# Performance work log

Measured on AMD Instinct MI355X. Metric: run time of the kernel, lower is better.

The kernel has to match this reference:

```python
import jax, jax.numpy as jnp
import numpy as np

B, IN, OUT = 65536, 256, 256
EPS = 1e-10


def setup_inputs() -> dict:
    key = jax.random.key(0)
    k1, k2, k3 = jax.random.split(key, 3)
    x = jax.random.normal(k1, (B, IN), dtype=jnp.float32)
    # match nn.Linear default init scale roughly (kaiming-uniform-ish)
    W = jax.random.normal(k2, (OUT, IN), dtype=jnp.float32) / np.sqrt(IN)
    b = jax.random.normal(k3, (OUT,), dtype=jnp.float32) / np.sqrt(IN)
    return {"x": x, "W": W, "b": b}


def reference(x, W, b):
    # x: [B, in], W: [out, in], b: [out]
    # x_len[i] = sqrt(sum_k x[i,k]^2)  (original does x^2 @ ones^T -> same value per out col)
    x_len = jnp.sqrt(jnp.sum(x * x, axis=-1, keepdims=True))           # [B, 1]
    # w_len[j] = sqrt(sum_k W[j,k]^2)  (original does ones @ (W^2)^T -> same value per row)
    w_len = jnp.sqrt(jnp.sum(W * W, axis=-1))[None, :]                  # [1, out]
    x_len = jax.lax.stop_gradient(x_len)
    w_len = jax.lax.stop_gradient(w_len)
    b_sg = jax.lax.stop_gradient(b)
    out = x @ W.T + b                                                   # linear(x), grads flow
    out = out - b_sg[None, :]                                           # bias.data subtraction (no grad)
    out = jnp.maximum(out / (x_len * w_len), EPS)                       # cosine normalize + clamp
    out = out + b_sg[None, :]                                           # bias.data added back (no grad)
    return out
```

## Files before the change

kernel.cpp:

```cpp
#include <hip/hip_runtime.h>
#include <hip/hip_bf16.h>
#include <math.h>


using bf16x8 = __attribute__((ext_vector_type(8))) short;
using f32x4  = __attribute__((ext_vector_type(4))) float;

#define W_LDS_BYTES 131072
#define LDS_BYTES   (W_LDS_BYTES + 1024 + 1024)
#define EPS 1e-10f

__device__ __forceinline__ short f2bf(float f) {
    __bf16 h = (__bf16)f;
    return __builtin_bit_cast(short, h);
}

__global__ __launch_bounds__(1024, 4) void ffn_cosnorm_kernel(
    const float* __restrict__ x, const float* __restrict__ W,
    const float* __restrict__ b, float* __restrict__ out)
{
    extern __shared__ char smem[];
    float* winv = (float*)(smem + W_LDS_BYTES);
    float* blds = (float*)(smem + W_LDS_BYTES + 1024);

    const int t    = threadIdx.x;
    const int lane = t & 63;
    const int wave = t >> 6;
    const int r16  = lane & 15;
    const int kg   = lane >> 4;
    const int rxor = (r16 & 7) << 4;
    const size_t rowb = (size_t)blockIdx.x * 256 + (size_t)wave * 16;

    const float* xp = x + (rowb + r16) * 256 + kg * 8;

    float4 fa[8], fb[8];
    #pragma unroll
    for (int s = 0; s < 8; ++s) {
        fa[s] = *(const float4*)(xp + s * 32);
        fb[s] = *(const float4*)(xp + s * 32 + 4);
    }

    {
        const int wrow = t >> 2;
        const int q    = t & 3;
        const float* wr = W + (size_t)wrow * 256 + q * 64;
        const int rx = (wrow & 7) << 4;
        float ss = 0.f;
        #pragma unroll
        for (int i = 0; i < 8; ++i) {
            float4 a = *(const float4*)(wr + i * 8);
            float4 c = *(const float4*)(wr + i * 8 + 4);
            ss = fmaf(a.x, a.x, ss); ss = fmaf(a.y, a.y, ss);
            ss = fmaf(a.z, a.z, ss); ss = fmaf(a.w, a.w, ss);
            ss = fmaf(c.x, c.x, ss); ss = fmaf(c.y, c.y, ss);
            ss = fmaf(c.z, c.z, ss); ss = fmaf(c.w, c.w, ss);
            bf16x8 v;
            v[0] = f2bf(a.x); v[1] = f2bf(a.y); v[2] = f2bf(a.z); v[3] = f2bf(a.w);
            v[4] = f2bf(c.x); v[5] = f2bf(c.y); v[6] = f2bf(c.z); v[7] = f2bf(c.w);
            const int off = wrow * 512 + ((q * 128 + i * 16) ^ rx);
            *(bf16x8*)(smem + off) = v;
        }
        ss += __shfl_xor(ss, 1);
        ss += __shfl_xor(ss, 2);
        if (q == 0) winv[wrow] = 1.0f / sqrtf(ss);
        if (t < 256) blds[t] = b[t];
    }

    bf16x8 xb[8];
    float ssx = 0.f;
    #pragma unroll
    for (int s = 0; s < 8; ++s) {
        float4 a = fa[s], c = fb[s];
        bf16x8 v;
        v[0] = f2bf(a.x); v[1] = f2bf(a.y); v[2] = f2bf(a.z); v[3] = f2bf(a.w);
        v[4] = f2bf(c.x); v[5] = f2bf(c.y); v[6] = f2bf(c.z); v[7] = f2bf(c.w);
        xb[s] = v;
        ssx = fmaf(a.x, a.x, ssx); ssx = fmaf(a.y, a.y, ssx);
        ssx = fmaf(a.z, a.z, ssx); ssx = fmaf(a.w, a.w, ssx);
        ssx = fmaf(c.x, c.x, ssx); ssx = fmaf(c.y, c.y, ssx);
        ssx = fmaf(c.z, c.z, ssx); ssx = fmaf(c.w, c.w, ssx);
    }

    ssx += __shfl_xor(ssx, 16); ssx += __shfl_xor(ssx, 32);
    const float inv = 1.0f / sqrtf(ssx);

    __syncthreads();

    const int jb = kg * 4;
    float* op = out + (rowb + r16) * 256;

    #pragma unroll
    for (int n = 0; n < 16; ++n) {
        f32x4 acc = f32x4{0.f, 0.f, 0.f, 0.f};
        #pragma unroll
        for (int k0 = 0; k0 < 8; ++k0) {
            const int addr = (n * 16 + r16) * 512 + ((k0 * 64 + kg * 16) ^ rxor);
            bf16x8 wfr = *(const bf16x8*)(smem + addr);
            acc = __builtin_amdgcn_mfma_f32_16x16x32_bf16(wfr, xb[k0], acc, 0, 0, 0);
        }
        float4 wv = *(const float4*)(winv + n * 16 + jb);
        float4 bv = *(const float4*)(blds + n * 16 + jb);
        f32x4 o;
        o[0] = fmaxf(acc[0] * (inv * wv.x), EPS) + bv.x;
        o[1] = fmaxf(acc[1] * (inv * wv.y), EPS) + bv.y;
        o[2] = fmaxf(acc[2] * (inv * wv.z), EPS) + bv.z;
        o[3] = fmaxf(acc[3] * (inv * wv.w), EPS) + bv.w;
        *(f32x4*)(op + n * 16 + jb) = o;
        __builtin_amdgcn_sched_barrier(0);
    }
}

extern "C" void kernel_launch(void* const* d_in, const int* in_sizes, int n_in,
                              void* d_out, int out_size, void* d_ws, size_t ws_size,
                              hipStream_t stream) {
    const float* x = (const float*)d_in[0];
    const float* W = (const float*)d_in[1];
    const float* b = (const float*)d_in[2];
    float* out = (float*)d_out;

    hipFuncSetAttribute((const void*)ffn_cosnorm_kernel,
                        hipFuncAttributeMaxDynamicSharedMemorySize, LDS_BYTES);
    ffn_cosnorm_kernel<<<dim3(256), dim3(1024), LDS_BYTES, stream>>>(x, W, b, out);
}
```

Before: 34.63 us.

## Split W staging into two K-halves to halve LDS and double block count

Blocks shrink from 1024 to 512 threads covering 128 rows each, and the bf16 copy of W is staged in two 64 KB halves along K instead of one 128 KB buffer. The first half feeds 16 accumulators kept in registers, then the second half is loaded and the norms and epilogue run. The smaller LDS footprint should let more blocks share a CU and doubles the grid to 512 blocks. In exchange every block reads and converts W twice with extra barriers, and holding 16 accumulator vectors raises register pressure. Waves also start at rotated column tiles to spread LDS bank traffic.

```diff
diff --git a/kernel.cpp b/kernel.cpp
--- a/kernel.cpp
+++ b/kernel.cpp
@@ -6,7 +6,7 @@
 using bf16x8 = __attribute__((ext_vector_type(8))) short;
 using f32x4  = __attribute__((ext_vector_type(4))) float;
 
-#define W_LDS_BYTES 131072
+#define W_LDS_BYTES 65536
 #define LDS_BYTES   (W_LDS_BYTES + 1024 + 1024)
 #define EPS 1e-10f
 
@@ -15,7 +15,7 @@
     return __builtin_bit_cast(short, h);
 }
 
-__global__ __launch_bounds__(1024, 4) void ffn_cosnorm_kernel(
+__global__ __launch_bounds__(512, 4) void ffn_cosnorm_kernel(
     const float* __restrict__ x, const float* __restrict__ W,
     const float* __restrict__ b, float* __restrict__ out)
 {
@@ -29,7 +29,7 @@
     const int r16  = lane & 15;
     const int kg   = lane >> 4;
     const int rxor = (r16 & 7) << 4;
-    const size_t rowb = (size_t)blockIdx.x * 256 + (size_t)wave * 16;
+    const size_t rowb = (size_t)blockIdx.x * 128 + (size_t)wave * 16;
 
     const float* xp = x + (rowb + r16) * 256 + kg * 8;
 
@@ -41,8 +41,8 @@
     }
 
     {
-        const int wrow = t >> 2;
-        const int q    = t & 3;
+        const int wrow = t >> 1;
+        const int q    = t & 1;
         const float* wr = W + (size_t)wrow * 256 + q * 64;
         const int rx = (wrow & 7) << 4;
         float ss = 0.f;
@@ -57,13 +57,12 @@
             bf16x8 v;
             v[0] = f2bf(a.x); v[1] = f2bf(a.y); v[2] = f2bf(a.z); v[3] = f2bf(a.w);
             v[4] = f2bf(c.x); v[5] = f2bf(c.y); v[6] = f2bf(c.z); v[7] = f2bf(c.w);
-            const int off = wrow * 512 + ((q * 128 + i * 16) ^ rx);
+            const int off = wrow * 256 + ((q * 128 + i * 16) ^ rx);
             *(bf16x8*)(smem + off) = v;
         }
         ss += __shfl_xor(ss, 1);
-        ss += __shfl_xor(ss, 2);
-        if (q == 0) winv[wrow] = 1.0f / sqrtf(ss);
-        if (t < 256) blds[t] = b[t];
+        if (!q) winv[wrow] = ss;
+        else    blds[wrow] = b[wrow];
     }
 
     bf16x8 xb[8];
@@ -80,31 +79,72 @@
         ssx = fmaf(c.x, c.x, ssx); ssx = fmaf(c.y, c.y, ssx);
         ssx = fmaf(c.z, c.z, ssx); ssx = fmaf(c.w, c.w, ssx);
     }
-
     ssx += __shfl_xor(ssx, 16); ssx += __shfl_xor(ssx, 32);
     const float inv = 1.0f / sqrtf(ssx);
 
     __syncthreads();
 
+    f32x4 acc[16];
+    #pragma unroll
+    for (int i = 0; i < 16; ++i) {
+        const int n = (wave * 2 + i) & 15;
+        f32x4 a = f32x4{0.f, 0.f, 0.f, 0.f};
+        #pragma unroll
+        for (int k0 = 0; k0 < 4; ++k0) {
+            const int addr = (n * 16 + r16) * 256 + ((k0 * 64 + kg * 16) ^ rxor);
+            bf16x8 wfr = *(const bf16x8*)(smem + addr);
+            a = __builtin_amdgcn_mfma_f32_16x16x32_bf16(wfr, xb[k0], a, 0, 0, 0);
+        }
+        acc[i] = a;
+    }
+
+    __syncthreads();
+
+    {
+        const int wrow = t >> 1;
+        const int q    = t & 1;
+        const float* wr = W + (size_t)wrow * 256 + 128 + q * 64;
+        const int rx = (wrow & 7) << 4;
+        float ss = 0.f;
+        #pragma unroll
+        for (int i = 0; i < 8; ++i) {
+            float4 a = *(const float4*)(wr + i * 8);
+            float4 c = *(const float4*)(wr + i * 8 + 4);
+            ss = fmaf(a.x, a.x, ss); ss = fmaf(a.y, a.y, ss);
+            ss = fmaf(a.z, a.z, ss); ss = fmaf(a.w, a.w, ss);
+            ss = fmaf(c.x, c.x, ss); ss = fmaf(c.y, c.y, ss);
+            ss = fmaf(c.z, c.z, ss); ss = fmaf(c.w, c.w, ss);
+            bf16x8 v;
+            v[0] = f2bf(a.x); v[1] = f2bf(a.y); v[2] = f2bf(a.z); v[3] = f2bf(a.w);
+            v[4] = f2bf(c.x); v[5] = f2bf(c.y); v[6] = f2bf(c.z); v[7] = f2bf(c.w);
+            const int off = wrow * 256 + ((q * 128 + i * 16) ^ rx);
+            *(bf16x8*)(smem + off) = v;
+        }
+        ss += __shfl_xor(ss, 1);
+        if (!q) winv[wrow] = 1.0f / sqrtf(winv[wrow] + ss);
+    }
+
+    __syncthreads();
+
     const int jb = kg * 4;
     float* op = out + (rowb + r16) * 256;
-
     #pragma unroll
-    for (int n = 0; n < 16; ++n) {
-        f32x4 acc = f32x4{0.f, 0.f, 0.f, 0.f};
+    for (int i = 0; i < 16; ++i) {
+        const int n = (wave * 2 + i) & 15;
+        f32x4 a = acc[i];
         #pragma unroll
-        for (int k0 = 0; k0 < 8; ++k0) {
-            const int addr = (n * 16 + r16) * 512 + ((k0 * 64 + kg * 16) ^ rxor);
+        for (int k0 = 0; k0 < 4; ++k0) {
+            const int addr = (n * 16 + r16) * 256 + ((k0 * 64 + kg * 16) ^ rxor);
             bf16x8 wfr = *(const bf16x8*)(smem + addr);
-            acc = __builtin_amdgcn_mfma_f32_16x16x32_bf16(wfr, xb[k0], acc, 0, 0, 0);
+            a = __builtin_amdgcn_mfma_f32_16x16x32_bf16(wfr, xb[4 + k0], a, 0, 0, 0);
         }
         float4 wv = *(const float4*)(winv + n * 16 + jb);
         float4 bv = *(const float4*)(blds + n * 16 + jb);
         f32x4 o;
-        o[0] = fmaxf(acc[0] * (inv * wv.x), EPS) + bv.x;
-        o[1] = fmaxf(acc[1] * (inv * wv.y), EPS) + bv.y;
-        o[2] = fmaxf(acc[2] * (inv * wv.z), EPS) + bv.z;
-        o[3] = fmaxf(acc[3] * (inv * wv.w), EPS) + bv.w;
+        o[0] = fmaxf(a[0] * (inv * wv.x), EPS) + bv.x;
+        o[1] = fmaxf(a[1] * (inv * wv.y), EPS) + bv.y;
+        o[2] = fmaxf(a[2] * (inv * wv.z), EPS) + bv.z;
+        o[3] = fmaxf(a[3] * (inv * wv.w), EPS) + bv.w;
         *(f32x4*)(op + n * 16 + jb) = o;
         __builtin_amdgcn_sched_barrier(0);
     }
@@ -120,5 +160,5 @@
 
     hipFuncSetAttribute((const void*)ffn_cosnorm_kernel,
                         hipFuncAttributeMaxDynamicSharedMemorySize, LDS_BYTES);
-    ffn_cosnorm_kernel<<<dim3(256), dim3(1024), LDS_BYTES, stream>>>(x, W, b, out);
+    ffn_cosnorm_kernel<<<dim3(512), dim3(512), LDS_BYTES, stream>>>(x, W, b, out);
 }
```

Result: slower. 45.01 us (+30.0%).

## Keep W in registers and stream x through double-buffered LDS slabs

Applied to the files above, without the earlier changes.

Each wave now holds two 16-column W slices as bf16 fragments in registers, and the x rows stream through two 8 KB LDS slabs, prefetching the next 16-row slab while the current one is used for MFMA. The grid becomes 512 blocks of 512 threads covering 128 rows each, cutting LDS from about 130 KB to about 16 KB per block, which allows more resident blocks. In exchange, every block re-reads and re-converts its W slices from global memory, and each slab step adds a block-wide barrier.

```diff
diff --git a/kernel.cpp b/kernel.cpp
--- a/kernel.cpp
+++ b/kernel.cpp
@@ -6,8 +6,8 @@
 using bf16x8 = __attribute__((ext_vector_type(8))) short;
 using f32x4  = __attribute__((ext_vector_type(4))) float;
 
-#define W_LDS_BYTES 131072
-#define LDS_BYTES   (W_LDS_BYTES + 1024 + 1024)
+#define SLAB_BYTES 8192
+#define LDS_BYTES  (2 * SLAB_BYTES + 2 * 16 * 4)
 #define EPS 1e-10f
 
 __device__ __forceinline__ short f2bf(float f) {
@@ -15,13 +15,27 @@
     return __builtin_bit_cast(short, h);
 }
 
-__global__ __launch_bounds__(1024, 4) void ffn_cosnorm_kernel(
+__device__ __forceinline__ float sumsq8(float4 a, float4 c, float s) {
+    s = fmaf(a.x, a.x, s); s = fmaf(a.y, a.y, s);
+    s = fmaf(a.z, a.z, s); s = fmaf(a.w, a.w, s);
+    s = fmaf(c.x, c.x, s); s = fmaf(c.y, c.y, s);
+    s = fmaf(c.z, c.z, s); s = fmaf(c.w, c.w, s);
+    return s;
+}
+
+__device__ __forceinline__ bf16x8 pack8(float4 a, float4 c) {
+    bf16x8 v;
+    v[0] = f2bf(a.x); v[1] = f2bf(a.y); v[2] = f2bf(a.z); v[3] = f2bf(a.w);
+    v[4] = f2bf(c.x); v[5] = f2bf(c.y); v[6] = f2bf(c.z); v[7] = f2bf(c.w);
+    return v;
+}
+
+__global__ __launch_bounds__(512, 4) void ffn_cosnorm_kernel(
     const float* __restrict__ x, const float* __restrict__ W,
     const float* __restrict__ b, float* __restrict__ out)
 {
     extern __shared__ char smem[];
-    float* winv = (float*)(smem + W_LDS_BYTES);
-    float* blds = (float*)(smem + W_LDS_BYTES + 1024);
+    float* ssq = (float*)(smem + 2 * SLAB_BYTES);
 
     const int t    = threadIdx.x;
     const int lane = t & 63;
@@ -29,84 +43,100 @@
     const int r16  = lane & 15;
     const int kg   = lane >> 4;
     const int rxor = (r16 & 7) << 4;
-    const size_t rowb = (size_t)blockIdx.x * 256 + (size_t)wave * 16;
+    const size_t rowbase = (size_t)blockIdx.x * 128;
 
-    const float* xp = x + (rowb + r16) * 256 + kg * 8;
+    const int srow = t >> 5;
+    const int c2   = t & 31;
+    const int soff = srow * 512 + ((c2 * 16) ^ ((srow & 7) << 4));
+    const float* sp = x + (rowbase + srow) * 256 + c2 * 8;
 
-    float4 fa[8], fb[8];
-    #pragma unroll
-    for (int s = 0; s < 8; ++s) {
-        fa[s] = *(const float4*)(xp + s * 32);
-        fb[s] = *(const float4*)(xp + s * 32 + 4);
+    float4 g0 = *(const float4*)(sp);
+    float4 g1 = *(const float4*)(sp + 4);
+
+    bf16x8 xw0[8], xw1[8];
+    float wv0[4], wv1[4];
+    float4 bv0, bv1;
+    const int n0 = wave, n1 = wave + 8;
+    {
+        const float* wr0 = W + (size_t)(n0 * 16 + r16) * 256 + kg * 8;
+        const float* wr1 = W + (size_t)(n1 * 16 + r16) * 256 + kg * 8;
+        float s0 = 0.f, s1 = 0.f;
+        #pragma unroll
+        for (int k0 = 0; k0 < 8; ++k0) {
+            float4 a0 = *(const float4*)(wr0 + k0 * 32);
+            float4 c0 = *(const float4*)(wr0 + k0 * 32 + 4);
+            xw0[k0] = pack8(a0, c0);
+            s0 = sumsq8(a0, c0, s0);
+            float4 a1 = *(const float4*)(wr1 + k0 * 32);
+            float4 c1 = *(const float4*)(wr1 + k0 * 32 + 4);
+            xw1[k0] = pack8(a1, c1);
+            s1 = sumsq8(a1, c1, s1);
+        }
+        s0 += __shfl_xor(s0, 16); s0 += __shfl_xor(s0, 32);
+        s1 += __shfl_xor(s1, 16); s1 += __shfl_xor(s1, 32);
+        const float iw0 = 1.0f / sqrtf(s0);
+        const float iw1 = 1.0f / sqrtf(s1);
+        #pragma unroll
+        for (int r = 0; r < 4; ++r) {
+            wv0[r] = __shfl(iw0, kg * 4 + r);
+            wv1[r] = __shfl(iw1, kg * 4 + r);
+        }
+        bv0 = *(const float4*)(b + n0 * 16 + kg * 4);
+        bv1 = *(const float4*)(b + n1 * 16 + kg * 4);
     }
 
     {
-        const int wrow = t >> 2;
-        const int q    = t & 3;
-        const float* wr = W + (size_t)wrow * 256 + q * 64;
-        const int rx = (wrow & 7) << 4;
-        float ss = 0.f;
-        #pragma unroll
-        for (int i = 0; i < 8; ++i) {
-            float4 a = *(const float4*)(wr + i * 8);
-            float4 c = *(const float4*)(wr + i * 8 + 4);
-            ss = fmaf(a.x, a.x, ss); ss = fmaf(a.y, a.y, ss);
-            ss = fmaf(a.z, a.z, ss); ss = fmaf(a.w, a.w, ss);
-            ss = fmaf(c.x, c.x, ss); ss = fmaf(c.y, c.y, ss);
-            ss = fmaf(c.z, c.z, ss); ss = fmaf(c.w, c.w, ss);
-            bf16x8 v;
-            v[0] = f2bf(a.x); v[1] = f2bf(a.y); v[2] = f2bf(a.z); v[3] = f2bf(a.w);
-            v[4] = f2bf(c.x); v[5] = f2bf(c.y); v[6] = f2bf(c.z); v[7] = f2bf(c.w);
-            const int off = wrow * 512 + ((q * 128 + i * 16) ^ rx);
-            *(bf16x8*)(smem + off) = v;
-        }
-        ss += __shfl_xor(ss, 1);
-        ss += __shfl_xor(ss, 2);
-        if (q == 0) winv[wrow] = 1.0f / sqrtf(ss);
-        if (t < 256) blds[t] = b[t];
+        float sp2 = sumsq8(g0, g1, 0.f);
+        *(bf16x8*)(smem + soff) = pack8(g0, g1);
+        sp2 += __shfl_xor(sp2, 1);  sp2 += __shfl_xor(sp2, 2);
+        sp2 += __shfl_xor(sp2, 4);  sp2 += __shfl_xor(sp2, 8);
+        sp2 += __shfl_xor(sp2, 16);
+        if ((lane & 31) == 0) ssq[srow] = sp2;
     }
-
-    bf16x8 xb[8];
-    float ssx = 0.f;
-    #pragma unroll
-    for (int s = 0; s < 8; ++s) {
-        float4 a = fa[s], c = fb[s];
-        bf16x8 v;
-        v[0] = f2bf(a.x); v[1] = f2bf(a.y); v[2] = f2bf(a.z); v[3] = f2bf(a.w);
-        v[4] = f2bf(c.x); v[5] = f2bf(c.y); v[6] = f2bf(c.z); v[7] = f2bf(c.w);
-        xb[s] = v;
-        ssx = fmaf(a.x, a.x, ssx); ssx = fmaf(a.y, a.y, ssx);
-        ssx = fmaf(a.z, a.z, ssx); ssx = fmaf(a.w, a.w, ssx);
-        ssx = fmaf(c.x, c.x, ssx); ssx = fmaf(c.y, c.y, ssx);
-        ssx = fmaf(c.z, c.z, ssx); ssx = fmaf(c.w, c.w, ssx);
-    }
-
-    ssx += __shfl_xor(ssx, 16); ssx += __shfl_xor(ssx, 32);
-    const float inv = 1.0f / sqrtf(ssx);
-
     __syncthreads();
 
-    const int jb = kg * 4;
-    float* op = out + (rowb + r16) * 256;
+    #pragma unroll
+    for (int i = 0; i < 8; ++i) {
+        const int cur = i & 1;
+        float4 h0, h1;
+        if (i < 7) {
+            const float* np = sp + (size_t)(i + 1) * 16 * 256;
+            h0 = *(const float4*)(np);
+            h1 = *(const float4*)(np + 4);
+        }
 
-    #pragma unroll
-    for (int n = 0; n < 16; ++n) {
-        f32x4 acc = f32x4{0.f, 0.f, 0.f, 0.f};
+        const float invx = 1.0f / sqrtf(ssq[cur * 16 + r16]);
+        f32x4 a0 = f32x4{0.f, 0.f, 0.f, 0.f};
+        f32x4 a1 = f32x4{0.f, 0.f, 0.f, 0.f};
         #pragma unroll
         for (int k0 = 0; k0 < 8; ++k0) {
-            const int addr = (n * 16 + r16) * 512 + ((k0 * 64 + kg * 16) ^ rxor);
-            bf16x8 wfr = *(const bf16x8*)(smem + addr);
-            acc = __builtin_amdgcn_mfma_f32_16x16x32_bf16(wfr, xb[k0], acc, 0, 0, 0);
+            bf16x8 bfr = *(const bf16x8*)(smem + cur * SLAB_BYTES +
+                                          r16 * 512 + ((k0 * 64 + kg * 16) ^ rxor));
+            a0 = __builtin_amdgcn_mfma_f32_16x16x32_bf16(xw0[k0], bfr, a0, 0, 0, 0);
+            a1 = __builtin_amdgcn_mfma_f32_16x16x32_bf16(xw1[k0], bfr, a1, 0, 0, 0);
         }
-        float4 wv = *(const float4*)(winv + n * 16 + jb);
-        float4 bv = *(const float4*)(blds + n * 16 + jb);
-        f32x4 o;
-        o[0] = fmaxf(acc[0] * (inv * wv.x), EPS) + bv.x;
-        o[1] = fmaxf(acc[1] * (inv * wv.y), EPS) + bv.y;
-        o[2] = fmaxf(acc[2] * (inv * wv.z), EPS) + bv.z;
-        o[3] = fmaxf(acc[3] * (inv * wv.w), EPS) + bv.w;
-        *(f32x4*)(op + n * 16 + jb) = o;
-        __builtin_amdgcn_sched_barrier(0);
+        float* op = out + (rowbase + i * 16 + r16) * 256;
+        f32x4 o0, o1;
+        o0[0] = fmaxf(a0[0] * (invx * wv0[0]), EPS) + bv0.x;
+        o0[1] = fmaxf(a0[1] * (invx * wv0[1]), EPS) + bv0.y;
+        o0[2] = fmaxf(a0[2] * (invx * wv0[2]), EPS) + bv0.z;
+        o0[3] = fmaxf(a0[3] * (invx * wv0[3]), EPS) + bv0.w;
+        o1[0] = fmaxf(a1[0] * (invx * wv1[0]), EPS) + bv1.x;
+        o1[1] = fmaxf(a1[1] * (invx * wv1[1]), EPS) + bv1.y;
+        o1[2] = fmaxf(a1[2] * (invx * wv1[2]), EPS) + bv1.z;
+        o1[3] = fmaxf(a1[3] * (invx * wv1[3]), EPS) + bv1.w;
+        *(f32x4*)(op + n0 * 16 + kg * 4) = o0;
+        *(f32x4*)(op + n1 * 16 + kg * 4) = o1;
+
+        if (i < 7) {
+            float sp2 = sumsq8(h0, h1, 0.f);
+            *(bf16x8*)(smem + (cur ^ 1) * SLAB_BYTES + soff) = pack8(h0, h1);
+            sp2 += __shfl_xor(sp2, 1);  sp2 += __shfl_xor(sp2, 2);
+            sp2 += __shfl_xor(sp2, 4);  sp2 += __shfl_xor(sp2, 8);
+            sp2 += __shfl_xor(sp2, 16);
+            if ((lane & 31) == 0) ssq[(cur ^ 1) * 16 + srow] = sp2;
+        }
+        __syncthreads();
     }
 }
 
@@ -120,5 +150,5 @@
 
     hipFuncSetAttribute((const void*)ffn_cosnorm_kernel,
                         hipFuncAttributeMaxDynamicSharedMemorySize, LDS_BYTES);
-    ffn_cosnorm_kernel<<<dim3(256), dim3(1024), LDS_BYTES, stream>>>(x, W, b, out);
+    ffn_cosnorm_kernel<<<dim3(512), dim3(512), LDS_BYTES, stream>>>(x, W, b, out);
 }
```

Measured after the change: 50.47 us. 1.46x slower.

## Stage x tiles through LDS with async global_load_lds double buffering

Applied to the files above, without the earlier changes.

Replaces direct per-thread register loads of x with asynchronous global-to-LDS DMA into a per-wave slab, double-buffered in 64-column quarters with XOR swizzling. Each wave waits on vmcnt, converts the staged quarter to bf16 and accumulates the norm while the next quarter streams in. The W staging now runs after an extra barrier because the x slabs reuse the W region of LDS. The per-tile sched_barrier in the output loop is also removed. This adds a barrier and serialises the x and W phases in exchange for coalesced DMA and lower register pressure.

```diff
diff --git a/kernel.cpp b/kernel.cpp
--- a/kernel.cpp
+++ b/kernel.cpp
@@ -13,6 +13,13 @@
 __device__ __forceinline__ short f2bf(float f) {
     __bf16 h = (__bf16)f;
     return __builtin_bit_cast(short, h);
+}
+
+__device__ __forceinline__ void dma16(const float* g, char* l) {
+    __builtin_amdgcn_global_load_lds(
+        (const __attribute__((address_space(1))) void*)g,
+        (__attribute__((address_space(3))) void*)l,
+        16 , 0, 0);
 }
 
 __global__ __launch_bounds__(1024, 4) void ffn_cosnorm_kernel(
@@ -31,14 +38,62 @@
     const int rxor = (r16 & 7) << 4;
     const size_t rowb = (size_t)blockIdx.x * 256 + (size_t)wave * 16;
 
-    const float* xp = x + (rowb + r16) * 256 + kg * 8;
+    char* slab = smem + wave * 8192;
 
-    float4 fa[8], fb[8];
+    const int drow = lane >> 4;
+    const int dc   = lane & 15;
+
     #pragma unroll
-    for (int s = 0; s < 8; ++s) {
-        fa[s] = *(const float4*)(xp + s * 32);
-        fb[s] = *(const float4*)(xp + s * 32 + 4);
+    for (int q = 0; q < 2; ++q) {
+        #pragma unroll
+        for (int j = 0; j < 4; ++j) {
+            const int row16 = j * 4 + drow;
+            const float* g = x + (rowb + row16) * 256 + q * 64
+                               + ((dc ^ (row16 & 7)) << 2);
+            dma16(g, slab + (q & 1) * 4096 + j * 1024);
+        }
     }
+
+    bf16x8 xb[8];
+    float ssx = 0.f;
+    #pragma unroll
+    for (int q = 0; q < 4; ++q) {
+        if (q < 3) asm volatile("s_waitcnt vmcnt(4)" ::: "memory");
+        else       asm volatile("s_waitcnt vmcnt(0)" ::: "memory");
+        __builtin_amdgcn_sched_barrier(0);
+        #pragma unroll
+        for (int k0 = 0; k0 < 2; ++k0) {
+            const int ch0 = (k0 * 8 + kg * 2) ^ (r16 & 7);
+            const int ch1 = (k0 * 8 + kg * 2 + 1) ^ (r16 & 7);
+            f32x4 a = *(const f32x4*)(slab + (q & 1) * 4096 + r16 * 256 + ch0 * 16);
+            f32x4 c = *(const f32x4*)(slab + (q & 1) * 4096 + r16 * 256 + ch1 * 16);
+            bf16x8 v;
+            v[0] = f2bf(a[0]); v[1] = f2bf(a[1]); v[2] = f2bf(a[2]); v[3] = f2bf(a[3]);
+            v[4] = f2bf(c[0]); v[5] = f2bf(c[1]); v[6] = f2bf(c[2]); v[7] = f2bf(c[3]);
+            xb[q * 2 + k0] = v;
+            ssx = fmaf(a[0], a[0], ssx); ssx = fmaf(a[1], a[1], ssx);
+            ssx = fmaf(a[2], a[2], ssx); ssx = fmaf(a[3], a[3], ssx);
+            ssx = fmaf(c[0], c[0], ssx); ssx = fmaf(c[1], c[1], ssx);
+            ssx = fmaf(c[2], c[2], ssx); ssx = fmaf(c[3], c[3], ssx);
+        }
+        if (q < 2) {
+            asm volatile("s_waitcnt lgkmcnt(0)" ::: "memory");
+            __builtin_amdgcn_sched_barrier(0);
+            const int nq = q + 2;
+            #pragma unroll
+            for (int j = 0; j < 4; ++j) {
+                const int row16 = j * 4 + drow;
+                const float* g = x + (rowb + row16) * 256 + nq * 64
+                                   + ((dc ^ (row16 & 7)) << 2);
+                dma16(g, slab + (nq & 1) * 4096 + j * 1024);
+            }
+        }
+    }
+
+    ssx += __shfl_xor(ssx, 16); ssx += __shfl_xor(ssx, 32);
+    const float inv = 1.0f / sqrtf(ssx);
+
+    __syncthreads();
 
     {
         const int wrow = t >> 2;
@@ -63,27 +118,8 @@
         ss += __shfl_xor(ss, 1);
         ss += __shfl_xor(ss, 2);
         if (q == 0) winv[wrow] = 1.0f / sqrtf(ss);
-        if (t < 256) blds[t] = b[t];
+        if (q == 1) blds[wrow] = b[wrow];
     }
-
-    bf16x8 xb[8];
-    float ssx = 0.f;
-    #pragma unroll
-    for (int s = 0; s < 8; ++s) {
-        float4 a = fa[s], c = fb[s];
-        bf16x8 v;
-        v[0] = f2bf(a.x); v[1] = f2bf(a.y); v[2] = f2bf(a.z); v[3] = f2bf(a.w);
-        v[4] = f2bf(c.x); v[5] = f2bf(c.y); v[6] = f2bf(c.z); v[7] = f2bf(c.w);
-        xb[s] = v;
-        ssx = fmaf(a.x, a.x, ssx); ssx = fmaf(a.y, a.y, ssx);
-        ssx = fmaf(a.z, a.z, ssx); ssx = fmaf(a.w, a.w, ssx);
-        ssx = fmaf(c.x, c.x, ssx); ssx = fmaf(c.y, c.y, ssx);
-        ssx = fmaf(c.z, c.z, ssx); ssx = fmaf(c.w, c.w, ssx);
-    }
-
-    ssx += __shfl_xor(ssx, 16); ssx += __shfl_xor(ssx, 32);
-    const float inv = 1.0f / sqrtf(ssx);
-
     __syncthreads();
 
     const int jb = kg * 4;
@@ -106,7 +142,6 @@
         o[2] = fmaxf(acc[2] * (inv * wv.z), EPS) + bv.z;
         o[3] = fmaxf(acc[3] * (inv * wv.w), EPS) + bv.w;
         *(f32x4*)(op + n * 16 + jb) = o;
-        __builtin_amdgcn_sched_barrier(0);
     }
 }
 
```

Result: slower. 35.65 us (+3.0%).
